# Kernel optimization log

Hardware: AMD Instinct MI355X
Metric: run time of the kernel (lower is better)

Reference implementation:

```python
import jax, jax.numpy as jnp
import numpy as np

E = 1024   # embedding_dim
H = 16     # heads
W = 1024   # lag / seq length
B = 4      # batch
D = E // H # head dim


def setup_inputs() -> dict:
    key = jax.random.key(0)
    ks = jax.random.split(key, 5)
    scale = E ** -0.5
    return {
        "x":   jax.random.normal(ks[0], (3, B, E, W), dtype=jnp.float32),
        "L_Q": jax.random.normal(ks[1], (E, E), dtype=jnp.float32) * scale,
        "L_K": jax.random.normal(ks[2], (E, E), dtype=jnp.float32) * scale,
        "L_V": jax.random.normal(ks[3], (E, E), dtype=jnp.float32) * scale,
        "M":   jax.random.normal(ks[4], (E, E), dtype=jnp.float32) * (1.0 / (2 * E)) ** 0.5,
        "b":   jnp.zeros((E, 1), dtype=jnp.float32),
    }


def reference(x, L_Q, L_K, L_V, M, b):
    # x: [3, B, E, W] channels-first; x[0]=K input, x[1]=Q input, x[2]=V input
    K = jnp.einsum('ef,bfw->bew', L_K, x[0])
    Q = jnp.einsum('ef,bfw->bew', L_Q, x[1])
    V = jnp.einsum('ef,bfw->bew', L_V, x[2])
    # reshape to [B, H, D, W]
    Kv = K.reshape(B, H, D, W)
    Qv = Q.reshape(B, H, D, W)
    Vv = V.reshape(B, H, D, W)
    # scores[b,h,q,k] = Q_v^T @ K_v
    scores = jnp.einsum('bhdq,bhdk->bhqk', Qv, Kv)
    # causal mask: -inf for q > k (strictly lower triangle), added BEFORE softmax
    q_idx = jnp.arange(W)[:, None]
    k_idx = jnp.arange(W)[None, :]
    mask = jnp.where(q_idx > k_idx, -jnp.inf, 0.0).astype(scores.dtype)
    scores = scores + mask
    # NON-STANDARD: softmax over the QUERY axis (dim=-2), then scale
    attn = jax.nn.softmax(scores, axis=-2) / (E ** 0.5)
    # V_v @ scores: [B,H,D,W] @ [B,H,W,W] -> [B,H,D,W]
    out = jnp.einsum('bhdq,bhqk->bhdk', Vv, attn).reshape(B, E, W)
    # dense: M @ out + b (dropout identity at inference)
    return jnp.einsum('oe,bew->bow', M, out) + b
```

## Files before the change

kernel.cpp:

```cpp
#include <hip/hip_runtime.h>
#include <stdint.h>
#include <math.h>

#define E_DIM 1024
#define W_DIM 1024
#define EW 1048576L

typedef _Float16 h16;
typedef __attribute__((ext_vector_type(8))) _Float16 h8;
typedef __attribute__((ext_vector_type(4))) float f4;

__device__ __forceinline__ void async_copy16(h16* lds, const h16* g) {
    __builtin_amdgcn_global_load_lds(
        (const __attribute__((address_space(1))) void*)g,
        (__attribute__((address_space(3))) void*)lds, 16, 0, 0);
}

__global__ __launch_bounds__(256) void prep(
    const float* __restrict__ x, const float* __restrict__ LK,
    const float* __restrict__ LQ, const float* __restrict__ LV,
    const float* __restrict__ Mw, h16* __restrict__ xt, h16* __restrict__ wh)
{
    __shared__ float Ts[64][65];
    const int z = blockIdx.z;
    const int t = threadIdx.x;
    if (z < 12) {
        const float* src = x + (long)z * EW;
        h16* dst = xt + (long)z * EW;
        const int e0 = blockIdx.y * 64, w0 = blockIdx.x * 64;
        const int r = t >> 4, c4 = (t & 15) * 4;
        #pragma unroll
        for (int p = 0; p < 4; ++p) {
            float4 v = *reinterpret_cast<const float4*>(src + (long)(e0 + r + p * 16) * W_DIM + w0 + c4);
            Ts[c4 + 0][r + p * 16] = v.x;
            Ts[c4 + 1][r + p * 16] = v.y;
            Ts[c4 + 2][r + p * 16] = v.z;
            Ts[c4 + 3][r + p * 16] = v.w;
        }
        __syncthreads();
        #pragma unroll
        for (int p = 0; p < 4; ++p) {
            int wr = r + p * 16;
            union { h16 h[4]; uint2 u; } o;
            o.h[0] = (h16)Ts[wr][c4 + 0];
            o.h[1] = (h16)Ts[wr][c4 + 1];
            o.h[2] = (h16)Ts[wr][c4 + 2];
            o.h[3] = (h16)Ts[wr][c4 + 3];
            *reinterpret_cast<uint2*>(dst + (long)(w0 + wr) * E_DIM + e0 + c4) = o.u;
        }
    } else {
        const float* srcs[4] = {LK, LQ, LV, Mw};
        const float* s = srcs[z - 12];
        h16* o = wh + (long)(z - 12) * EW;
        long base = ((long)(blockIdx.y * 16 + blockIdx.x)) * 1024 + t;
        #pragma unroll
        for (int k = 0; k < 4; ++k) {
            long i = base + k * 256;
            float4 v = reinterpret_cast<const float4*>(s)[i];
            union { h16 h[4]; uint2 u; } u;
            u.h[0] = (h16)v.x; u.h[1] = (h16)v.y; u.h[2] = (h16)v.z; u.h[3] = (h16)v.w;
            reinterpret_cast<uint2*>(o)[i] = u.u;
        }
    }
}

__global__ __launch_bounds__(512) void gemm_proj3(
    const h16* __restrict__ xh, const h16* __restrict__ Wts,
    h16* __restrict__ KQV)
{
    __shared__ h16 As[2][256 * 64];
    __shared__ h16 Bs[2][256 * 64];

    const int t = threadIdx.x;
    const int wave = t >> 6, lane = t & 63;
    const int quad = lane >> 4, l16 = lane & 15;
    const int mi = wave >> 2, ni = wave & 3;
    const int wm = mi * 128, wn = ni * 64;

    const int lin = (int)blockIdx.x + ((int)blockIdx.y << 2) + ((int)blockIdx.z << 4);
    const int swz = (lin & 7) * 24 + (lin >> 3);
    const int bx = swz & 3, by = (swz >> 2) & 3, zz = swz >> 4;

    const int m0 = by * 256, n0 = bx * 256;

    const int proj = zz >> 2, bz = zz & 3;
    const h16 *A, *Bt; h16* C;
    if (proj == 0)      { A = xh + bz * EW;       Bt = Wts;          C = KQV + bz * EW; }
    else if (proj == 1) { A = xh + (4 + bz) * EW; Bt = Wts + EW;     C = KQV + (4 + bz) * EW; }
    else                { A = Wts + 2 * EW;       Bt = xh + (8 + bz) * EW; C = KQV + (8 + bz) * EW; }

    f4 acc[8][4] = {};

    auto stage = [&](int buf, int k0) {
        #pragma unroll
        for (int j = 0; j < 4; ++j) {
            int g = j * 512 + t, row = g >> 3, cg = (g & 7) ^ (row & 7);
            async_copy16(&As[buf][g * 8], A  + (long)(m0 + row) * E_DIM + k0 + cg * 8);
            async_copy16(&Bs[buf][g * 8], Bt + (long)(n0 + row) * E_DIM + k0 + cg * 8);
        }
    };

    stage(0, 0);

    for (int T = 0; T < 16; ++T) {
        if (T + 1 < 16) {
            stage((T + 1) & 1, (T + 1) * 64);
            asm volatile("s_waitcnt vmcnt(8)" ::: "memory");
        } else {
            asm volatile("s_waitcnt vmcnt(0)" ::: "memory");
        }
        __builtin_amdgcn_s_barrier();

        const h16* as = As[T & 1];
        const h16* bs = Bs[T & 1];

        #pragma unroll
        for (int c = 0; c < 2; ++c) {
            h8 bv[4];
            #pragma unroll
            for (int j = 0; j < 4; ++j) {
                int rb = wn + j * 16 + l16;
                bv[j] = *reinterpret_cast<const h8*>(&bs[(rb * 8 + ((c * 4 + quad) ^ (l16 & 7))) * 8]);
            }
            #pragma unroll
            for (int fh = 0; fh < 2; ++fh) {
                h8 av[4];
                #pragma unroll
                for (int i = 0; i < 4; ++i) {
                    int ra = wm + fh * 64 + i * 16 + l16;
                    av[i] = *reinterpret_cast<const h8*>(&as[(ra * 8 + ((c * 4 + quad) ^ (l16 & 7))) * 8]);
                }
                __builtin_amdgcn_s_setprio(1);
                #pragma unroll
                for (int i = 0; i < 4; ++i)
                    #pragma unroll
                    for (int j = 0; j < 4; ++j)
                        acc[fh * 4 + i][j] = __builtin_amdgcn_mfma_f32_16x16x32_f16(av[i], bv[j], acc[fh * 4 + i][j], 0, 0, 0);
                __builtin_amdgcn_s_setprio(0);
            }
        }
        __builtin_amdgcn_s_barrier();
    }

    #pragma unroll
    for (int mt = 0; mt < 8; ++mt)
        #pragma unroll
        for (int i = 0; i < 4; ++i) {
            int m = m0 + wm + mt * 16 + quad * 4 + i;
            #pragma unroll
            for (int nt = 0; nt < 4; ++nt)
                C[(long)m * W_DIM + n0 + wn + nt * 16 + l16] = (h16)acc[mt][nt][i];
        }
}

__global__ __launch_bounds__(256) void gemm_out(
    const h16* __restrict__ A, const h16* __restrict__ Bt,
    float* __restrict__ C, const float* __restrict__ bias)
{
    __shared__ h16 As[64 * 64];
    __shared__ h16 Bs[128 * 64];

    const int t = threadIdx.x;
    const int wave = t >> 6, lane = t & 63;
    const int quad = lane >> 4, l16 = lane & 15;
    const int m0 = blockIdx.y * 64, n0 = blockIdx.x * 128;
    const int wm = (wave >> 1) * 32, wn = (wave & 1) * 64;

    f4 acc[2][4] = {};

    for (int k0 = 0; k0 < 1024; k0 += 64) {
        __syncthreads();
        #pragma unroll
        for (int j = 0; j < 2; ++j) {
            int g = j * 256 + t, row = g >> 3, cg = (g & 7) ^ (row & 7);
            async_copy16(&As[g * 8], A + (long)(m0 + row) * E_DIM + k0 + cg * 8);
        }
        #pragma unroll
        for (int j = 0; j < 4; ++j) {
            int g = j * 256 + t, row = g >> 3, cg = (g & 7) ^ (row & 7);
            async_copy16(&Bs[g * 8], Bt + (long)(n0 + row) * E_DIM + k0 + cg * 8);
        }
        __syncthreads();

        h8 av[2][2], bv[4][2];
        #pragma unroll
        for (int c = 0; c < 2; ++c) {
            #pragma unroll
            for (int mt = 0; mt < 2; ++mt) {
                int r = wm + mt * 16 + l16;
                av[mt][c] = *reinterpret_cast<const h8*>(&As[(r * 8 + ((c * 4 + quad) ^ (l16 & 7))) * 8]);
            }
            #pragma unroll
            for (int nt = 0; nt < 4; ++nt) {
                int r = wn + nt * 16 + l16;
                bv[nt][c] = *reinterpret_cast<const h8*>(&Bs[(r * 8 + ((c * 4 + quad) ^ (l16 & 7))) * 8]);
            }
        }
        #pragma unroll
        for (int c = 0; c < 2; ++c)
            #pragma unroll
            for (int mt = 0; mt < 2; ++mt)
                #pragma unroll
                for (int nt = 0; nt < 4; ++nt)
                    acc[mt][nt] = __builtin_amdgcn_mfma_f32_16x16x32_f16(av[mt][c], bv[nt][c], acc[mt][nt], 0, 0, 0);
    }

    #pragma unroll
    for (int mt = 0; mt < 2; ++mt)
        #pragma unroll
        for (int i = 0; i < 4; ++i) {
            int m = m0 + wm + mt * 16 + quad * 4 + i;
            float bv_ = bias ? bias[m] : 0.f;
            #pragma unroll
            for (int nt = 0; nt < 4; ++nt) {
                int n = n0 + wn + nt * 16 + l16;
                C[(long)(n >> 10) * EW + (long)m * W_DIM + (n & 1023)] = acc[mt][nt][i] + bv_;
            }
        }
}

__global__ __launch_bounds__(512) void attn_mfma(
    const h16* __restrict__ Kt, const h16* __restrict__ Qt,
    const h16* __restrict__ V, h16* __restrict__ AoT)
{
    __shared__ h16 Qs[2][64 * 64];
    __shared__ h16 Vs[2][64 * 64];
    __shared__ h16 Ps[8][16 * 64];

    const int t = threadIdx.x, wave = t >> 6, lane = t & 63;
    const int quad = lane >> 4, l16 = lane & 15;
    const int y = blockIdx.y;
    const int b = y >> 4, h = y & 15;
    const int cxor = (y & 7) ^ (((y >> 5) & 1) ? 7 : 0);
    const int ktb = (int)blockIdx.x ^ cxor;
    const int nit = 2 * ktb + 2;
    const int kwave = ktb * 128 + wave * 16;
    const int kc = kwave + l16;

    const h16* Ktb_ = Kt + (long)b * EW + h * 64;
    const h16* Qtb  = Qt + (long)b * EW + h * 64;
    const h16* Vb   = V  + (long)b * EW + (long)(h * 64) * W_DIM;
    h16* Pw = &Ps[wave][0];

    h8 kb0 = *reinterpret_cast<const h8*>(Ktb_ + (long)kc * E_DIM + quad * 8);
    h8 kb1 = *reinterpret_cast<const h8*>(Ktb_ + (long)kc * E_DIM + 32 + quad * 8);

    {
        int row = t >> 3, cg = (t & 7) ^ (row & 7);
        async_copy16(&Qs[0][t * 8], Qtb + (long)row * E_DIM + cg * 8);
        async_copy16(&Vs[0][t * 8], Vb + (long)row * W_DIM + cg * 8);
    }

    const float L2E = 1.442695041f;
    float mr = -1e30f, ls = 0.f;
    f4 O[4] = {};

    for (int it = 0; it < nit; ++it) {
        const int q0 = it * 64;
        __syncthreads();
        if (it + 1 < nit) {
            const int nb = (it + 1) & 1, q1 = q0 + 64;
            int row = t >> 3, cg = (t & 7) ^ (row & 7);
            async_copy16(&Qs[nb][t * 8], Qtb + (long)(q1 + row) * E_DIM + cg * 8);
            async_copy16(&Vs[nb][t * 8], Vb + (long)row * W_DIM + q1 + cg * 8);
        }
        if (q0 > kwave + 15) continue;

        const h16* qs = Qs[it & 1];
        const h16* vs = Vs[it & 1];

        f4 S[4];
        __builtin_amdgcn_s_setprio(1);
        #pragma unroll
        for (int nt = 0; nt < 4; ++nt) {
            int row = nt * 16 + l16;
            h8 a0 = *reinterpret_cast<const h8*>(&qs[(row * 8 + (quad ^ (l16 & 7))) * 8]);
            h8 a1 = *reinterpret_cast<const h8*>(&qs[(row * 8 + ((4 + quad) ^ (l16 & 7))) * 8]);
            f4 s = {};
            s = __builtin_amdgcn_mfma_f32_16x16x32_f16(a0, kb0, s, 0, 0, 0);
            s = __builtin_amdgcn_mfma_f32_16x16x32_f16(a1, kb1, s, 0, 0, 0);
            S[nt] = s;
        }
        __builtin_amdgcn_s_setprio(0);

        if (it >= 2 * ktb) {
            #pragma unroll
            for (int nt = 0; nt < 4; ++nt)
                #pragma unroll
                for (int i = 0; i < 4; ++i)
                    if (q0 + nt * 16 + quad * 4 + i > kc) S[nt][i] = -1e30f;
        }

        float mx = -1e30f;
        #pragma unroll
        for (int nt = 0; nt < 4; ++nt) {
            float t0 = fmaxf(fmaxf(S[nt][0], S[nt][1]), fmaxf(S[nt][2], S[nt][3]));
            mx = fmaxf(mx, t0);
        }
        mx = fmaxf(mx, __shfl_xor(mx, 16));
        mx = fmaxf(mx, __shfl_xor(mx, 32));

        if (__any(mx - mr > 8.f)) {
            float nm = fmaxf(mr, mx);
            float al = exp2f((mr - nm) * L2E);
            mr = nm;
            ls *= al;
            #pragma unroll
            for (int dt = 0; dt < 4; ++dt)
                #pragma unroll
                for (int i = 0; i < 4; ++i) O[dt][i] *= al;
        }

        const float mc = mr * L2E;
        float tsa = 0.f, tsb = 0.f;
        #pragma unroll
        for (int nt = 0; nt < 4; ++nt)
            #pragma unroll
            for (int i = 0; i < 4; ++i) {
                float p = exp2f(fmaf(S[nt][i], L2E, -mc));
                S[nt][i] = p;
                if (i & 1) tsb += p; else tsa += p;
            }
        float ts = tsa + tsb;
        ts += __shfl_xor(ts, 16);
        ts += __shfl_xor(ts, 32);
        ls += ts;

        #pragma unroll
        for (int nt = 0; nt < 4; ++nt) {
            int sg = ((nt * 2 + (quad >> 1)) ^ (l16 & 7)) * 8 + (quad & 1) * 4;
            union { h16 hh[4]; uint2 u2; } u0;
            #pragma unroll
            for (int i = 0; i < 4; ++i) u0.hh[i] = (h16)S[nt][i];
            *reinterpret_cast<uint2*>(Pw + l16 * 64 + sg) = u0.u2;
        }
        asm volatile("" ::: "memory");

        __builtin_amdgcn_s_setprio(1);
        #pragma unroll
        for (int c = 0; c < 2; ++c) {
            int sg = ((c * 4 + quad) ^ (l16 & 7)) * 8;
            h8 pb = *reinterpret_cast<const h8*>(Pw + l16 * 64 + sg);
            #pragma unroll
            for (int dt = 0; dt < 4; ++dt) {
                int r = dt * 16 + l16;
                h8 va = *reinterpret_cast<const h8*>(&vs[(r * 8 + ((c * 4 + quad) ^ (l16 & 7))) * 8]);
                O[dt] = __builtin_amdgcn_mfma_f32_16x16x32_f16(va, pb, O[dt], 0, 0, 0);
            }
        }
        __builtin_amdgcn_s_setprio(0);
    }

    const float inv = 0.03125f / ls;
    #pragma unroll
    for (int dt = 0; dt < 4; ++dt) {
        int sg = ((dt * 2 + (quad >> 1)) ^ (l16 & 7)) * 8 + (quad & 1) * 4;
        union { h16 hh[4]; uint2 u2; } u0;
        #pragma unroll
        for (int i = 0; i < 4; ++i) u0.hh[i] = (h16)(O[dt][i] * inv);
        *reinterpret_cast<uint2*>(Pw + l16 * 64 + sg) = u0.u2;
    }
    asm volatile("" ::: "memory");
    #pragma unroll
    for (int j = 0; j < 2; ++j) {
        int sg = ((quad * 2 + j) ^ (l16 & 7)) * 8;
        uint4 vv = *reinterpret_cast<const uint4*>(Pw + l16 * 64 + sg);
        *reinterpret_cast<uint4*>(AoT + (long)b * EW + (long)(kwave + l16) * E_DIM
                                  + h * 64 + quad * 16 + j * 8) = vv;
    }
}

extern "C" void kernel_launch(void* const* d_in, const int* in_sizes, int n_in,
                              void* d_out, int out_size, void* d_ws, size_t ws_size,
                              hipStream_t stream)
{
    const float* x  = (const float*)d_in[0];
    const float* LQ = (const float*)d_in[1];
    const float* LK = (const float*)d_in[2];
    const float* LV = (const float*)d_in[3];
    const float* Mw = (const float*)d_in[4];
    const float* bb = (const float*)d_in[5];
    float* out = (float*)d_out;
    h16* ws = (h16*)d_ws;

    h16* xh  = ws;
    h16* LKh = ws + 12 * EW;
    h16* Mh  = ws + 15 * EW;
    h16* Kp  = ws + 16 * EW;
    h16* Qp  = ws + 20 * EW;
    h16* Vp  = ws + 24 * EW;
    h16* Ao  = ws + 28 * EW;

    dim3 blk(256);
    prep<<<dim3(16, 16, 16), blk, 0, stream>>>(x, LK, LQ, LV, Mw, xh, LKh);
    gemm_proj3<<<dim3(4, 4, 12), dim3(512), 0, stream>>>(xh, LKh, Kp);
    attn_mfma<<<dim3(8, 64), dim3(512), 0, stream>>>(Kp, Qp, Vp, Ao);
    gemm_out<<<dim3(32, 16), blk, 0, stream>>>(Mh, Ao, out, bb);
}
```

Before: 190.8 us.

## Deepen projection GEMM pipeline to four K=32 stages with interleaved A/B loads

Restructures the QKV projection GEMM main loop from double-buffered K=64 tiles into a 4-deep ring of K=32 tiles. The A and B async loads for a future stage are issued at separate points, interleaved with two half-tile MFMA phases, and vmcnt waits are tuned per iteration. The LDS swizzle changes to match the 32-wide rows. The goal is to keep more loads in flight and hide memory latency behind MFMA work. In exchange there are more barriers per unit of K, and the waitcnt bookkeeping is fragile.

```diff
diff --git a/kernel.cpp b/kernel.cpp
--- a/kernel.cpp
+++ b/kernel.cpp
@@ -68,8 +68,8 @@
     const h16* __restrict__ xh, const h16* __restrict__ Wts,
     h16* __restrict__ KQV)
 {
-    __shared__ h16 As[2][256 * 64];
-    __shared__ h16 Bs[2][256 * 64];
+    __shared__ h16 As[4][256 * 32];
+    __shared__ h16 Bs[4][256 * 32];
 
     const int t = threadIdx.x;
     const int wave = t >> 6, lane = t & 63;
@@ -91,54 +91,72 @@
 
     f4 acc[8][4] = {};
 
-    auto stage = [&](int buf, int k0) {
+    auto stageA = [&](int buf, int k0) {
+        #pragma unroll
+        for (int j = 0; j < 2; ++j) {
+            int g = j * 512 + t, row = g >> 2, cg = (g & 3) ^ ((row >> 1) & 3);
+            async_copy16(&As[buf][g * 8], A + (long)(m0 + row) * E_DIM + k0 + cg * 8);
+        }
+    };
+    auto stageB = [&](int buf, int k0) {
+        #pragma unroll
+        for (int j = 0; j < 2; ++j) {
+            int g = j * 512 + t, row = g >> 2, cg = (g & 3) ^ ((row >> 1) & 3);
+            async_copy16(&Bs[buf][g * 8], Bt + (long)(n0 + row) * E_DIM + k0 + cg * 8);
+        }
+    };
+
+    stageA(0, 0);  stageB(0, 0);
+    stageA(1, 32); stageB(1, 32);
+    stageA(2, 64); stageB(2, 64);
+    asm volatile("s_waitcnt vmcnt(8)" ::: "memory");
+    __builtin_amdgcn_s_barrier();
+
+    for (int H = 0; H < 32; ++H) {
+        const h16* as = As[H & 3];
+        const h16* bs = Bs[H & 3];
+        const int kn = (H + 3) * 32;
+        const bool st = (H + 3) < 32;
+
+        h8 bv[4], av[4];
         #pragma unroll
         for (int j = 0; j < 4; ++j) {
-            int g = j * 512 + t, row = g >> 3, cg = (g & 7) ^ (row & 7);
-            async_copy16(&As[buf][g * 8], A  + (long)(m0 + row) * E_DIM + k0 + cg * 8);
-            async_copy16(&Bs[buf][g * 8], Bt + (long)(n0 + row) * E_DIM + k0 + cg * 8);
-        }
-    };
-
-    stage(0, 0);
-
-    for (int T = 0; T < 16; ++T) {
-        if (T + 1 < 16) {
-            stage((T + 1) & 1, (T + 1) * 64);
-            asm volatile("s_waitcnt vmcnt(8)" ::: "memory");
-        } else {
-            asm volatile("s_waitcnt vmcnt(0)" ::: "memory");
-        }
+            int rb = wn + j * 16 + l16;
+            bv[j] = *reinterpret_cast<const h8*>(&bs[(rb * 4 + (quad ^ ((rb >> 1) & 3))) * 8]);
+        }
+        #pragma unroll
+        for (int i = 0; i < 4; ++i) {
+            int ra = wm + i * 16 + l16;
+            av[i] = *reinterpret_cast<const h8*>(&as[(ra * 4 + (quad ^ ((ra >> 1) & 3))) * 8]);
+        }
+        if (st) stageA((H + 3) & 3, kn);
         __builtin_amdgcn_s_barrier();
-
-        const h16* as = As[T & 1];
-        const h16* bs = Bs[T & 1];
-
-        #pragma unroll
-        for (int c = 0; c < 2; ++c) {
-            h8 bv[4];
-            #pragma unroll
-            for (int j = 0; j < 4; ++j) {
-                int rb = wn + j * 16 + l16;
-                bv[j] = *reinterpret_cast<const h8*>(&bs[(rb * 8 + ((c * 4 + quad) ^ (l16 & 7))) * 8]);
-            }
-            #pragma unroll
-            for (int fh = 0; fh < 2; ++fh) {
-                h8 av[4];
-                #pragma unroll
-                for (int i = 0; i < 4; ++i) {
-                    int ra = wm + fh * 64 + i * 16 + l16;
-                    av[i] = *reinterpret_cast<const h8*>(&as[(ra * 8 + ((c * 4 + quad) ^ (l16 & 7))) * 8]);
-                }
-                __builtin_amdgcn_s_setprio(1);
-                #pragma unroll
-                for (int i = 0; i < 4; ++i)
-                    #pragma unroll
-                    for (int j = 0; j < 4; ++j)
-                        acc[fh * 4 + i][j] = __builtin_amdgcn_mfma_f32_16x16x32_f16(av[i], bv[j], acc[fh * 4 + i][j], 0, 0, 0);
-                __builtin_amdgcn_s_setprio(0);
-            }
-        }
+        __builtin_amdgcn_s_setprio(1);
+        #pragma unroll
+        for (int i = 0; i < 4; ++i)
+            #pragma unroll
+            for (int j = 0; j < 4; ++j)
+                acc[i][j] = __builtin_amdgcn_mfma_f32_16x16x32_f16(av[i], bv[j], acc[i][j], 0, 0, 0);
+        __builtin_amdgcn_s_setprio(0);
+        __builtin_amdgcn_s_barrier();
+
+        #pragma unroll
+        for (int i = 0; i < 4; ++i) {
+            int ra = wm + 64 + i * 16 + l16;
+            av[i] = *reinterpret_cast<const h8*>(&as[(ra * 4 + (quad ^ ((ra >> 1) & 3))) * 8]);
+        }
+        if (st) stageB((H + 3) & 3, kn);
+        if (H < 29)       asm volatile("s_waitcnt vmcnt(8)" ::: "memory");
+        else if (H == 29) asm volatile("s_waitcnt vmcnt(4)" ::: "memory");
+        else if (H == 30) asm volatile("s_waitcnt vmcnt(0)" ::: "memory");
+        __builtin_amdgcn_s_barrier();
+        __builtin_amdgcn_s_setprio(1);
+        #pragma unroll
+        for (int i = 0; i < 4; ++i)
+            #pragma unroll
+            for (int j = 0; j < 4; ++j)
+                acc[4 + i][j] = __builtin_amdgcn_mfma_f32_16x16x32_f16(av[i], bv[j], acc[4 + i][j], 0, 0, 0);
+        __builtin_amdgcn_s_setprio(0);
         __builtin_amdgcn_s_barrier();
     }
 
```

Result: no change. 188.7 us (-1.1%).
